# Performance work log

Hardware: AMD Instinct MI355X
Metric: run time of the kernel (lower is better)

The kernel has to match this reference:

```python
import jax, jax.numpy as jnp
import numpy as np

B, T, C, H = 4, 2048, 1024, 16
D = C // H  # head_size = 64


def setup_inputs() -> dict:
    key = jax.random.key(0)
    k1, k2, k3 = jax.random.split(key, 3)
    h = jax.random.normal(k1, (B, T, C), dtype=jnp.float32)
    # additive float mask, [B,1,1,T]; zeros = no padding
    attention_mask = jnp.zeros((B, 1, 1, T), dtype=jnp.float32)
    # learned params (bias=False linears), scaled like default torch init
    w_attn = jax.random.normal(k2, (C, 3 * C), dtype=jnp.float32) / np.sqrt(C)
    w_proj = jax.random.normal(k3, (C, C), dtype=jnp.float32) / np.sqrt(C)
    return {"h": h, "attention_mask": attention_mask, "w_attn": w_attn, "w_proj": w_proj}


def reference(h, attention_mask, w_attn, w_proj):
    # fused QKV projection: [B,T,3C]
    qkv = jnp.einsum("btc,cd->btd", h, w_attn)
    q, k, v = jnp.split(qkv, 3, axis=-1)
    # [B,T,C] -> [B,H,T,D]
    def to_heads(x):
        return x.reshape(B, T, H, D).transpose(0, 2, 1, 3)
    q, k, v = to_heads(q), to_heads(k), to_heads(v)
    # scaled dot-product attention with additive mask (non-causal)
    scale = 1.0 / np.sqrt(D).astype(np.float32)
    scores = jnp.einsum("bhqd,bhkd->bhqk", q, k) * scale + attention_mask
    probs = jax.nn.softmax(scores, axis=-1)
    y = jnp.einsum("bhqk,bhkd->bhqd", probs, v)
    # [B,H,T,D] -> [B,T,C]
    y = y.transpose(0, 2, 1, 3).reshape(B, T, C)
    return jnp.einsum("btc,cd->btd", y, w_proj)
```

## Files before the change

kernel.cpp:

```cpp
#include <hip/hip_runtime.h>
#include <hip/hip_bf16.h>

#define DEV static __device__ __forceinline__

typedef __attribute__((ext_vector_type(4))) float f32x4;
typedef __attribute__((ext_vector_type(8))) short bf16x8;

constexpr int Bb = 4, Ts = 2048, Cc = 1024, Hh = 16, Dd = 64;
constexpr int Mm = Bb * Ts;
constexpr float SCQ = 0.18033688f;

union frag_u {
  bf16x8 f;
  uint2  u2[2];
  ushort us[8];
  uint4  u4;
};

DEV ushort f2bf(float x) {
  union { float f; unsigned u; } v; v.f = x;
  unsigned r = v.u + 0x7FFFu + ((v.u >> 16) & 1u);
  return (ushort)(r >> 16);
}

DEV ushort f2bf_hw(float x) {
  union { __hip_bfloat16 b; ushort u; } cv;
  cv.b = __float2bfloat16(x);
  return cv.u;
}

typedef const __attribute__((address_space(1))) unsigned int gu32;
typedef __attribute__((address_space(3))) unsigned int lu32;
DEV void gload16(const void* g, void* l) {
  __builtin_amdgcn_global_load_lds((gu32*)g, (lu32*)l, 16, 0, 0);
}

DEV void lds_st128(ushort* lds, int row, int c16, uint4 v) {
  int off = row * 128 + ((c16 ^ (row & 7)) << 4);
  *reinterpret_cast<uint4*>(reinterpret_cast<char*>(lds) + off) = v;
}
DEV void ld_frag16(frag_u& fr, const ushort* lds, int row, int chunk) {
  int off = row * 128 + ((chunk ^ (row & 7)) << 4);
  fr.u4 = *reinterpret_cast<const uint4*>(reinterpret_cast<const char*>(lds) + off);
}
DEV void lds_st64p(ushort* lds, int row, int p, uint2 v) {
  int off = row * 128 + ((((p >> 3) ^ (row & 7)) << 4) | ((2 * p) & 15));
  *reinterpret_cast<uint2*>(reinterpret_cast<char*>(lds) + off) = v;
}

__global__ __launch_bounds__(256) void cvt_kernel(const float* __restrict__ in,
                                                  ushort* __restrict__ out, int n4) {
  for (int i = blockIdx.x * blockDim.x + threadIdx.x; i < n4;
       i += gridDim.x * blockDim.x) {
    float4 v = reinterpret_cast<const float4*>(in)[i];
    ushort4 o;
    o.x = f2bf(v.x); o.y = f2bf(v.y); o.z = f2bf(v.z); o.w = f2bf(v.w);
    reinterpret_cast<ushort4*>(out)[i] = o;
  }
}

__global__ __launch_bounds__(256) void transpose_cvt(const float* __restrict__ in,
                                                     ushort* __restrict__ out,
                                                     int R, int Ccols) {
  __shared__ float tile[32][33];
  int c0 = blockIdx.x * 32, r0 = blockIdx.y * 32;
  int tx = threadIdx.x & 31, ty = threadIdx.x >> 5;
#pragma unroll
  for (int i = 0; i < 4; ++i) {
    int r = ty + i * 8;
    tile[r][tx] = in[(size_t)(r0 + r) * Ccols + c0 + tx];
  }
  __syncthreads();
#pragma unroll
  for (int i = 0; i < 4; ++i) {
    int r = ty + i * 8;
    out[(size_t)(c0 + r) * R + r0 + tx] = f2bf(tile[tx][r]);
  }
}

template <int EPI>
__global__ __launch_bounds__(256) void gemm_bt(const ushort* __restrict__ A,
                                               const ushort* __restrict__ Bt,
                                               int M, int N, int K,
                                               float* __restrict__ Cf,
                                               ushort* __restrict__ Qb,
                                               ushort* __restrict__ Kb,
                                               ushort* __restrict__ Vb,
                                               const float* __restrict__ maskp) {
  __shared__ ushort Al[128 * 64];
  __shared__ ushort Bl[128 * 64];
  const int tid = threadIdx.x;
  const int lane = tid & 63, wid = tid >> 6;
  const int g = lane >> 4, l15 = lane & 15;
  const int wr = wid >> 1, wc = wid & 1;
  const int m0 = blockIdx.y * 128, n0 = blockIdx.x * 128;

  f32x4 acc[4][4];
#pragma unroll
  for (int i = 0; i < 4; ++i)
#pragma unroll
    for (int j = 0; j < 4; ++j) acc[i][j] = f32x4{0.f, 0.f, 0.f, 0.f};

  const int nkt = K >> 6;
  for (int kt = 0; kt < nkt; ++kt) {
#pragma unroll
    for (int it = 0; it < 4; ++it) {
      int chunk = wid * 256 + it * 64 + lane;
      int row = chunk >> 3, p = chunk & 7;
      int c16 = p ^ (row & 7);
      gload16(A + (size_t)(m0 + row) * K + kt * 64 + c16 * 8,
              Al + (size_t)(wid * 256 + it * 64) * 8);
      gload16(Bt + (size_t)(n0 + row) * K + kt * 64 + c16 * 8,
              Bl + (size_t)(wid * 256 + it * 64) * 8);
    }
    __syncthreads();
#pragma unroll
    for (int ks = 0; ks < 2; ++ks) {
      frag_u af[4], bfr[4];
#pragma unroll
      for (int i = 0; i < 4; ++i) {
        ld_frag16(af[i], Al, wr * 64 + i * 16 + l15, 4 * ks + g);
        ld_frag16(bfr[i], Bl, wc * 64 + i * 16 + l15, 4 * ks + g);
      }
#pragma unroll
      for (int i = 0; i < 4; ++i)
#pragma unroll
        for (int j = 0; j < 4; ++j)
          acc[i][j] = __builtin_amdgcn_mfma_f32_16x16x32_bf16(af[i].f, bfr[j].f,
                                                              acc[i][j], 0, 0, 0);
    }
    __syncthreads();
  }

#pragma unroll
  for (int i = 0; i < 4; ++i)
#pragma unroll
    for (int j = 0; j < 4; ++j) {
      int mrow = m0 + wr * 64 + i * 16 + 4 * g;
      int ncol = n0 + wc * 64 + j * 16 + l15;
#pragma unroll
      for (int r = 0; r < 4; ++r) {
        float v = acc[i][j][r];
        int m = mrow + r;
        if (EPI == 0) {
          Cf[(size_t)m * N + ncol] = v;
        } else {
          int which = ncol >> 10, c = ncol & 1023;
          int hd = c >> 6, d = c & 63;
          int b = m >> 11, t = m & 2047;
          size_t idx;
          if (which == 2) {
            v *= __expf(maskp[(size_t)b * Ts + t]);
            idx = (((size_t)(b * Hh + hd)) * Dd + d) * Ts + t;
          } else {
            if (which == 0) v *= SCQ;
            idx = (((size_t)(b * Hh + hd)) * Ts + t) * Dd + d;
          }
          ushort bv = f2bf(v);
          ushort* dst = (which == 0) ? Qb : (which == 1) ? Kb : Vb;
          dst[idx] = bv;
        }
      }
    }
}

__global__ __launch_bounds__(512, 4) void attn_kernel(const ushort* __restrict__ Qb,
                                                      const ushort* __restrict__ Kb,
                                                      const ushort* __restrict__ VTb,
                                                      const float* __restrict__ mask,
                                                      ushort* __restrict__ Yb) {
  __shared__ ushort Klds[2][64 * 64];
  __shared__ ushort Vlds[2][64 * 64];
  __shared__ ushort wlds[2][64];

  const int tid = threadIdx.x;
  const int lane = tid & 63, wid = tid >> 6;
  const int g = lane >> 4, l15 = lane & 15;
  const int bh = blockIdx.x;
  const int b = bh >> 4, h = bh & 15;
  const int qt = blockIdx.y;

  const ushort* Qh = Qb + (size_t)bh * Ts * Dd;
  const ushort* Kh = Kb + (size_t)bh * Ts * Dd;
  const ushort* Vh = VTb + (size_t)bh * Dd * Ts;
  const float* mrow = mask + (size_t)b * Ts;

  const int krow = tid >> 3, kpos = tid & 7;
  const int kc16 = kpos ^ (krow & 7);
  const int srow = tid >> 3, sc16 = tid & 7;
  const int vp0 = 32 * (sc16 >> 2) + 16 * (sc16 & 1) + 4 * ((sc16 >> 1) & 1);
  const int wp = (tid & 32) | ((tid & 12) << 1) | ((tid & 16) >> 2) | (tid & 3);

  frag_u aq[2][2];
#pragma unroll
  for (int qsub = 0; qsub < 2; ++qsub) {
    const ushort* qp = Qh + (size_t)(qt * 256 + wid * 32 + qsub * 16 + l15) * Dd;
#pragma unroll
    for (int ks = 0; ks < 2; ++ks)
      aq[qsub][ks].u4 = *reinterpret_cast<const uint4*>(qp + ks * 32 + 8 * g);
  }

  f32x4 acc[2][4];
  f32x4 lacc[2];
#pragma unroll
  for (int q = 0; q < 2; ++q) {
    lacc[q] = f32x4{0.f, 0.f, 0.f, 0.f};
#pragma unroll
    for (int dt = 0; dt < 4; ++dt) acc[q][dt] = f32x4{0.f, 0.f, 0.f, 0.f};
  }

  uint4 vreg;
  float wreg = 0.f;

#define ISSUE(kt, buf)                                                          \
  gload16(Kh + (size_t)((kt) * 64 + krow) * Dd + kc16 * 8,                      \
          Klds[buf] + (size_t)(wid * 64) * 8);                                  \
  vreg = *reinterpret_cast<const uint4*>(Vh + (size_t)srow * Ts + (kt) * 64 + sc16 * 8); \
  wreg = (tid < 64) ? __expf(mrow[(kt) * 64 + tid]) : 0.f;

#define COMMIT(buf)                                                             \
  lds_st64p(Vlds[buf], srow, vp0, uint2{vreg.x, vreg.y});                       \
  lds_st64p(Vlds[buf], srow, vp0 + 8, uint2{vreg.z, vreg.w});                   \
  if (tid < 64) wlds[buf][wp] = f2bf_hw(wreg);

  ISSUE(0, 0);
  COMMIT(0);
  __syncthreads();

  const int NT = Ts / 64;
  for (int kt = 0; kt < NT; ++kt) {
    const int cur = kt & 1;
    const bool more = (kt + 1 < NT);
    if (more) { ISSUE(kt + 1, cur ^ 1); }

    f32x4 s[2][4];
#pragma unroll
    for (int q = 0; q < 2; ++q)
#pragma unroll
      for (int n = 0; n < 4; ++n) s[q][n] = f32x4{0.f, 0.f, 0.f, 0.f};
    __builtin_amdgcn_s_setprio(1);
#pragma unroll
    for (int ks = 0; ks < 2; ++ks)
#pragma unroll
      for (int n = 0; n < 4; ++n) {
        frag_u bk;
        ld_frag16(bk, Klds[cur], n * 16 + l15, 4 * ks + g);
#pragma unroll
        for (int q = 0; q < 2; ++q)
          s[q][n] = __builtin_amdgcn_mfma_f32_16x16x32_bf16(bk.f, aq[q][ks].f,
                                                            s[q][n], 0, 0, 0);
      }
    __builtin_amdgcn_s_setprio(0);

    frag_u pa[2][2];
#pragma unroll
    for (int q = 0; q < 2; ++q)
#pragma unroll
      for (int n = 0; n < 4; ++n)
#pragma unroll
        for (int r = 0; r < 4; ++r)
          pa[q][n >> 1].us[(n & 1) * 4 + r] =
              f2bf_hw(__builtin_amdgcn_exp2f(s[q][n][r]));

    frag_u wf[2];
    wf[0].u4 = *reinterpret_cast<const uint4*>(&wlds[cur][8 * g]);
    wf[1].u4 = *reinterpret_cast<const uint4*>(&wlds[cur][32 + 8 * g]);
    __builtin_amdgcn_s_setprio(1);
#pragma unroll
    for (int ks = 0; ks < 2; ++ks)
#pragma unroll
      for (int q = 0; q < 2; ++q)
        lacc[q] = __builtin_amdgcn_mfma_f32_16x16x32_bf16(pa[q][ks].f, wf[ks].f,
                                                          lacc[q], 0, 0, 0);
#pragma unroll
    for (int ks = 0; ks < 2; ++ks)
#pragma unroll
      for (int dt = 0; dt < 4; ++dt) {
        frag_u bv;
        ld_frag16(bv, Vlds[cur], dt * 16 + l15, 4 * ks + g);
#pragma unroll
        for (int q = 0; q < 2; ++q)
          acc[q][dt] = __builtin_amdgcn_mfma_f32_16x16x32_bf16(pa[q][ks].f, bv.f,
                                                               acc[q][dt], 0, 0, 0);
      }
    __builtin_amdgcn_s_setprio(0);

    if (more) { COMMIT(cur ^ 1); }
    __syncthreads();
  }
#undef ISSUE
#undef COMMIT

#pragma unroll
  for (int q = 0; q < 2; ++q) {
#pragma unroll
    for (int r = 0; r < 4; ++r) {
      float inv = 1.0f / lacc[q][r];
      int t = qt * 256 + wid * 32 + q * 16 + 4 * g + r;
      size_t base = ((size_t)(b * Ts + t)) * Cc + h * Dd;
#pragma unroll
      for (int dt = 0; dt < 4; ++dt)
        Yb[base + dt * 16 + l15] = f2bf(acc[q][dt][r] * inv);
    }
  }
}

extern "C" void kernel_launch(void* const* d_in, const int* in_sizes, int n_in,
                              void* d_out, int out_size, void* d_ws, size_t ws_size,
                              hipStream_t stream) {
  const float* h    = (const float*)d_in[0];
  const float* mask = (const float*)d_in[1];
  const float* wa   = (const float*)d_in[2];
  const float* wp   = (const float*)d_in[3];
  float* out = (float*)d_out;

  char* ws = (char*)d_ws;
  ushort* hbf     = (ushort*)(ws);
  ushort* wattn_t = (ushort*)(ws + (16u << 20));
  ushort* wproj_t = (ushort*)(ws + (22u << 20));
  ushort* Qb      = (ushort*)(ws + (24u << 20));
  ushort* Kb      = (ushort*)(ws + (40u << 20));
  ushort* VTb     = (ushort*)(ws + (56u << 20));
  ushort* Ybf = hbf;

  cvt_kernel<<<2048, 256, 0, stream>>>(h, hbf, (Mm * Cc) / 4);
  transpose_cvt<<<dim3(3 * Cc / 32, Cc / 32), 256, 0, stream>>>(wa, wattn_t, Cc, 3 * Cc);
  transpose_cvt<<<dim3(Cc / 32, Cc / 32), 256, 0, stream>>>(wp, wproj_t, Cc, Cc);

  gemm_bt<1><<<dim3(3 * Cc / 128, Mm / 128), 256, 0, stream>>>(
      hbf, wattn_t, Mm, 3 * Cc, Cc, nullptr, Qb, Kb, VTb, mask);

  attn_kernel<<<dim3(Bb * Hh, Ts / 256), 512, 0, stream>>>(Qb, Kb, VTb, mask, Ybf);

  gemm_bt<0><<<dim3(Cc / 128, Mm / 128), 256, 0, stream>>>(
      Ybf, wproj_t, Mm, Cc, Cc, out, nullptr, nullptr, nullptr, nullptr);
}
```

Measured before the change: 195.6 us.

## Add 256x256 pipelined QKV GEMM and double-buffer output projection GEMM

Replaces the 128x128 QKV projection GEMM with a dedicated 256x256-tile kernel using 512 threads. It double-buffers LDS with staggered async global-to-LDS loads interleaved with MFMA phases, and adds setprio and a block-index swizzle for L2 locality. The output projection GEMM also gets double-buffered LDS so the next tile loads while the current one computes. The goal is to hide global load latency and raise MFMA utilisation, at the cost of more LDS (128KB per block in the QKV kernel) and lower occupancy.

```diff
diff --git a/kernel.cpp b/kernel.cpp
--- a/kernel.cpp
+++ b/kernel.cpp
@@ -35,10 +35,6 @@
   __builtin_amdgcn_global_load_lds((gu32*)g, (lu32*)l, 16, 0, 0);
 }
 
-DEV void lds_st128(ushort* lds, int row, int c16, uint4 v) {
-  int off = row * 128 + ((c16 ^ (row & 7)) << 4);
-  *reinterpret_cast<uint4*>(reinterpret_cast<char*>(lds) + off) = v;
-}
 DEV void ld_frag16(frag_u& fr, const ushort* lds, int row, int chunk) {
   int off = row * 128 + ((chunk ^ (row & 7)) << 4);
   fr.u4 = *reinterpret_cast<const uint4*>(reinterpret_cast<const char*>(lds) + off);
@@ -78,23 +74,145 @@
   }
 }
 
-template <int EPI>
+__global__ __launch_bounds__(512, 2) void gemm256_qkv(const ushort* __restrict__ A,
+                                                      const ushort* __restrict__ Bt,
+                                                      ushort* __restrict__ Qb,
+                                                      ushort* __restrict__ Kb,
+                                                      ushort* __restrict__ Vb,
+                                                      const float* __restrict__ maskp) {
+  __shared__ ushort Lds[2][4][128 * 64];
+  const int tid = threadIdx.x;
+  const int lane = tid & 63, wid = tid >> 6;
+  const int g = lane >> 4, l15 = lane & 15;
+  const int wm = wid >> 2, wn = wid & 3;
+
+  const int flat = blockIdx.y * 12 + blockIdx.x;
+  const int swz = (flat & 7) * 48 + (flat >> 3);
+  const int bx = swz % 12, by = swz / 12;
+  const int m0 = by * 256, n0 = bx * 256;
+  constexpr int K = 1024, nkt = K / 64;
+
+#define STAGE(slot, region, gbase, gRow0, kt)                                   \
+  {                                                                             \
+    _Pragma("unroll") for (int i = 0; i < 2; ++i) {                             \
+      int q = wid * 128 + i * 64 + lane;                                        \
+      int row = q >> 3, c = (q & 7) ^ (row & 7);                                \
+      gload16((gbase) + (size_t)((gRow0) + row) * K + (kt) * 64 + c * 8,        \
+              &Lds[slot][region][(size_t)(wid * 128 + i * 64) * 8]);            \
+    }                                                                           \
+  }
+
+  f32x4 acc[8][4];
+#pragma unroll
+  for (int i = 0; i < 8; ++i)
+#pragma unroll
+    for (int j = 0; j < 4; ++j) acc[i][j] = f32x4{0.f, 0.f, 0.f, 0.f};
+
+  STAGE(0, 0, A, m0, 0);
+  STAGE(0, 1, A, m0 + 128, 0);
+  STAGE(0, 2, Bt, n0, 0);
+  STAGE(0, 3, Bt, n0 + 128, 0);
+  STAGE(1, 2, Bt, n0, 1);
+  STAGE(1, 3, Bt, n0 + 128, 1);
+  asm volatile("s_waitcnt vmcnt(4)" ::: "memory");
+  __builtin_amdgcn_s_barrier();
+
+  frag_u bf[4][2];
+  for (int t = 0; t < nkt; ++t) {
+    const int s = t & 1;
+    const ushort* Acur = Lds[s][wm];
+    const ushort* Bcur = Lds[s][2 + (wn >> 1)];
+    const int browb = (wn & 1) * 64;
+
+#pragma unroll
+    for (int p = 0; p < 4; ++p) {
+      frag_u af[2][2];
+#pragma unroll
+      for (int m2 = 0; m2 < 2; ++m2)
+#pragma unroll
+        for (int ks = 0; ks < 2; ++ks)
+          ld_frag16(af[m2][ks], Acur, (2 * p + m2) * 16 + l15, 4 * ks + g);
+      if (p == 0) {
+#pragma unroll
+        for (int n = 0; n < 4; ++n)
+#pragma unroll
+          for (int ks = 0; ks < 2; ++ks)
+            ld_frag16(bf[n][ks], Bcur, browb + n * 16 + l15, 4 * ks + g);
+        if (t + 1 < nkt) STAGE((t + 1) & 1, 0, A, m0, t + 1);
+      }
+      if (p == 1 && t + 2 < nkt) STAGE(s, 2, Bt, n0, t + 2);
+      if (p == 2 && t + 1 < nkt) STAGE((t + 1) & 1, 1, A, m0 + 128, t + 1);
+      if (p == 3 && t + 2 < nkt) STAGE(s, 3, Bt, n0 + 128, t + 2);
+
+      __builtin_amdgcn_s_barrier();
+      asm volatile("s_waitcnt lgkmcnt(0)" ::: "memory");
+      __builtin_amdgcn_sched_barrier(0);
+      __builtin_amdgcn_s_setprio(1);
+#pragma unroll
+      for (int m2 = 0; m2 < 2; ++m2)
+#pragma unroll
+        for (int n = 0; n < 4; ++n)
+#pragma unroll
+          for (int ks = 0; ks < 2; ++ks)
+            acc[2 * p + m2][n] = __builtin_amdgcn_mfma_f32_16x16x32_bf16(
+                af[m2][ks].f, bf[n][ks].f, acc[2 * p + m2][n], 0, 0, 0);
+      __builtin_amdgcn_s_setprio(0);
+      __builtin_amdgcn_sched_barrier(0);
+      if (p == 3) asm volatile("s_waitcnt vmcnt(2)" ::: "memory");
+      __builtin_amdgcn_s_barrier();
+    }
+  }
+#undef STAGE
+
+  asm volatile("s_waitcnt vmcnt(0)" ::: "memory");
+
+  const int seg = bx >> 2;
+  ushort* dst = (seg == 0) ? Qb : (seg == 1) ? Kb : Vb;
+#pragma unroll
+  for (int mi = 0; mi < 8; ++mi) {
+#pragma unroll
+    for (int r = 0; r < 4; ++r) {
+      int mrow = m0 + wm * 128 + mi * 16 + 4 * g + r;
+      int b = mrow >> 11, tt = mrow & 2047;
+      float vs = (seg == 2) ? __expf(maskp[(size_t)b * Ts + tt])
+                            : (seg == 0 ? SCQ : 1.f);
+#pragma unroll
+      for (int n = 0; n < 4; ++n) {
+        int col = (bx & 3) * 256 + wn * 64 + n * 16 + l15;
+        int hd = col >> 6, d = col & 63;
+        size_t idx = (seg == 2)
+            ? (((size_t)(b * Hh + hd)) * Dd + d) * Ts + tt
+            : (((size_t)(b * Hh + hd)) * Ts + tt) * Dd + d;
+        dst[idx] = f2bf(acc[mi][n][r] * vs);
+      }
+    }
+  }
+}
+
 __global__ __launch_bounds__(256) void gemm_bt(const ushort* __restrict__ A,
                                                const ushort* __restrict__ Bt,
                                                int M, int N, int K,
-                                               float* __restrict__ Cf,
-                                               ushort* __restrict__ Qb,
-                                               ushort* __restrict__ Kb,
-                                               ushort* __restrict__ Vb,
-                                               const float* __restrict__ maskp) {
-  __shared__ ushort Al[128 * 64];
-  __shared__ ushort Bl[128 * 64];
+                                               float* __restrict__ Cf) {
+  __shared__ ushort Al[2][128 * 64];
+  __shared__ ushort Bl[2][128 * 64];
   const int tid = threadIdx.x;
   const int lane = tid & 63, wid = tid >> 6;
   const int g = lane >> 4, l15 = lane & 15;
   const int wr = wid >> 1, wc = wid & 1;
   const int m0 = blockIdx.y * 128, n0 = blockIdx.x * 128;
 
+#define ISSUE(slot, kt)                                                         \
+  {                                                                             \
+    _Pragma("unroll") for (int it = 0; it < 4; ++it) {                          \
+      int chunk = wid * 256 + it * 64 + lane;                                   \
+      int row = chunk >> 3, c16 = (chunk & 7) ^ (row & 7);                      \
+      gload16(A + (size_t)(m0 + row) * K + (kt) * 64 + c16 * 8,                 \
+              Al[slot] + (size_t)(wid * 256 + it * 64) * 8);                    \
+      gload16(Bt + (size_t)(n0 + row) * K + (kt) * 64 + c16 * 8,                \
+              Bl[slot] + (size_t)(wid * 256 + it * 64) * 8);                    \
+    }                                                                           \
+  }
+
   f32x4 acc[4][4];
 #pragma unroll
   for (int i = 0; i < 4; ++i)
@@ -102,25 +220,18 @@
     for (int j = 0; j < 4; ++j) acc[i][j] = f32x4{0.f, 0.f, 0.f, 0.f};
 
   const int nkt = K >> 6;
+  ISSUE(0, 0);
+  __syncthreads();
   for (int kt = 0; kt < nkt; ++kt) {
-#pragma unroll
-    for (int it = 0; it < 4; ++it) {
-      int chunk = wid * 256 + it * 64 + lane;
-      int row = chunk >> 3, p = chunk & 7;
-      int c16 = p ^ (row & 7);
-      gload16(A + (size_t)(m0 + row) * K + kt * 64 + c16 * 8,
-              Al + (size_t)(wid * 256 + it * 64) * 8);
-      gload16(Bt + (size_t)(n0 + row) * K + kt * 64 + c16 * 8,
-              Bl + (size_t)(wid * 256 + it * 64) * 8);
-    }
-    __syncthreads();
+    const int s = kt & 1;
+    if (kt + 1 < nkt) ISSUE(s ^ 1, kt + 1);
 #pragma unroll
     for (int ks = 0; ks < 2; ++ks) {
       frag_u af[4], bfr[4];
 #pragma unroll
       for (int i = 0; i < 4; ++i) {
-        ld_frag16(af[i], Al, wr * 64 + i * 16 + l15, 4 * ks + g);
-        ld_frag16(bfr[i], Bl, wc * 64 + i * 16 + l15, 4 * ks + g);
+        ld_frag16(af[i], Al[s], wr * 64 + i * 16 + l15, 4 * ks + g);
+        ld_frag16(bfr[i], Bl[s], wc * 64 + i * 16 + l15, 4 * ks + g);
       }
 #pragma unroll
       for (int i = 0; i < 4; ++i)
@@ -131,6 +242,7 @@
     }
     __syncthreads();
   }
+#undef ISSUE
 
 #pragma unroll
   for (int i = 0; i < 4; ++i)
@@ -139,28 +251,8 @@
       int mrow = m0 + wr * 64 + i * 16 + 4 * g;
       int ncol = n0 + wc * 64 + j * 16 + l15;
 #pragma unroll
-      for (int r = 0; r < 4; ++r) {
-        float v = acc[i][j][r];
-        int m = mrow + r;
-        if (EPI == 0) {
-          Cf[(size_t)m * N + ncol] = v;
-        } else {
-          int which = ncol >> 10, c = ncol & 1023;
-          int hd = c >> 6, d = c & 63;
-          int b = m >> 11, t = m & 2047;
-          size_t idx;
-          if (which == 2) {
-            v *= __expf(maskp[(size_t)b * Ts + t]);
-            idx = (((size_t)(b * Hh + hd)) * Dd + d) * Ts + t;
-          } else {
-            if (which == 0) v *= SCQ;
-            idx = (((size_t)(b * Hh + hd)) * Ts + t) * Dd + d;
-          }
-          ushort bv = f2bf(v);
-          ushort* dst = (which == 0) ? Qb : (which == 1) ? Kb : Vb;
-          dst[idx] = bv;
-        }
-      }
+      for (int r = 0; r < 4; ++r)
+        Cf[(size_t)(mrow + r) * N + ncol] = acc[i][j][r];
     }
 }
 
@@ -327,11 +419,10 @@
   transpose_cvt<<<dim3(3 * Cc / 32, Cc / 32), 256, 0, stream>>>(wa, wattn_t, Cc, 3 * Cc);
   transpose_cvt<<<dim3(Cc / 32, Cc / 32), 256, 0, stream>>>(wp, wproj_t, Cc, Cc);
 
-  gemm_bt<1><<<dim3(3 * Cc / 128, Mm / 128), 256, 0, stream>>>(
-      hbf, wattn_t, Mm, 3 * Cc, Cc, nullptr, Qb, Kb, VTb, mask);
+  gemm256_qkv<<<dim3(12, 32), 512, 0, stream>>>(hbf, wattn_t, Qb, Kb, VTb, mask);
 
   attn_kernel<<<dim3(Bb * Hh, Ts / 256), 512, 0, stream>>>(Qb, Kb, VTb, mask, Ybf);
 
-  gemm_bt<0><<<dim3(Cc / 128, Mm / 128), 256, 0, stream>>>(
-      Ybf, wproj_t, Mm, Cc, Cc, out, nullptr, nullptr, nullptr, nullptr);
-}
+  gemm_bt<<<dim3(Cc / 128, Mm / 128), 256, 0, stream>>>(
+      Ybf, wproj_t, Mm, Cc, Cc, out);
+}
```

Result: no change. 199.0 us (+1.7%).
